# Optimization experiments

Hardware: AMD Instinct MI355X
Metric: run time of the kernel (lower is better)

## Reference

```python
import jax, jax.numpy as jnp
import numpy as np
from jax import lax

K = 7          # kernel size
G = 12         # groups
EPS = 1e-5


def bn(x, gamma, beta, axes):
    # training-mode batch norm (torch default train() mode uses batch stats)
    mean = jnp.mean(x, axis=axes, keepdims=True)
    var = jnp.var(x, axis=axes, keepdims=True)
    shape = [1] * x.ndim
    shape[1 if x.ndim == 4 else -1] = -1
    g = gamma.reshape(shape)
    b = beta.reshape(shape)
    return g * (x - mean) * lax.rsqrt(var + EPS) + b


def setup_inputs() -> dict:
    key = jax.random.key(0)
    ks = jax.random.split(key, 12)
    B, C, H, Wd = 16, 192, 32, 32
    Cr = C // 4                      # reduce_mapping out channels = out_channels // reduce_ratio = 48
    flat = C * H * Wd                # 196608
    inp = {
        "x": jax.random.normal(ks[0], (B, C, H, Wd), jnp.float32),
        "Wr": jax.random.normal(ks[1], (Cr, C), jnp.float32) * 0.05,          # reduce_mapping 1x1 conv
        "gamma_s": jnp.ones((Cr,), jnp.float32),
        "beta_s": jnp.zeros((Cr,), jnp.float32),
        "Ws": jax.random.normal(ks[2], (K * K * G, Cr), jnp.float32) * 0.05,  # span_mapping 1x1 conv
        "W1": jax.random.normal(ks[3], (512, flat), jnp.float32) * 0.002,
        "b1": jnp.zeros((512,), jnp.float32),
        "g1": jnp.ones((512,), jnp.float32),
        "beta1": jnp.zeros((512,), jnp.float32),
        "W2": jax.random.normal(ks[4], (128, 512), jnp.float32) * 0.04,
        "b2": jnp.zeros((128,), jnp.float32),
        "g2": jnp.ones((128,), jnp.float32),
        "beta2": jnp.zeros((128,), jnp.float32),
        "W3": jax.random.normal(ks[5], (17, 128), jnp.float32) * 0.09,
        "b3": jnp.zeros((17,), jnp.float32),
    }
    return inp


def reference(x, Wr, gamma_s, beta_s, Ws, W1, b1, g1, beta1, W2, b2, g2, beta2, W3, b3):
    B, C, H, Wd = x.shape
    Cg = C // G
    # unfold (im2col) with kernel 7, pad 3, stride 1, dil 1 -> [B, C*K*K, H, W]
    # channel ordering (c, kh, kw) matches torch.nn.Unfold
    patches = lax.conv_general_dilated_patches(x, (K, K), (1, 1), [(K // 2, K // 2)] * 2)
    unf = patches.reshape(B, G, Cg, K * K, H, Wd)
    # kernel generation path: 1x1 reduce conv -> BN+ReLU -> 1x1 span conv
    red = jnp.einsum('bchw,oc->bohw', x, Wr)
    red = jax.nn.relu(bn(red, gamma_s, beta_s, (0, 2, 3)))
    ker = jnp.einsum('bchw,oc->bohw', red, Ws).reshape(B, G, K * K, H, Wd)
    # involution: per-pixel kernel multiply + sum over K*K
    out = jnp.einsum('bgkhw,bgckhw->bgchw', ker, unf).reshape(B, C, H, Wd)
    # classifier head
    flat = out.reshape(B, -1)
    h = jax.nn.relu(bn(flat @ W1.T + b1, g1, beta1, (0,)))
    h = jax.nn.relu(bn(h @ W2.T + b2, g2, beta2, (0,)))
    return h @ W3.T + b3
```

## Files before the change

kernel.cpp:

```cpp
#include <hip/hip_runtime.h>

#define EPS 1e-5f

typedef float v4f __attribute__((ext_vector_type(4)));

__global__ __launch_bounds__(256) void k_reduce_conv(
    const float* __restrict__ x, const float* __restrict__ Wr,
    float* __restrict__ red, float* __restrict__ spart)
{
  int ob = blockIdx.x >> 6;
  int pb = blockIdx.x & 63;
  int o0 = ob * 6;
  int pix = (pb << 8) + threadIdx.x;
  int b = pix >> 10;
  int hw = pix & 1023;
  const float* xp = x + ((size_t)b * 192) * 1024 + hw;
  float acc[6] = {0.f, 0.f, 0.f, 0.f, 0.f, 0.f};
  for (int c = 0; c < 192; ++c) {
    float xv = xp[(size_t)c * 1024];
#pragma unroll
    for (int j = 0; j < 6; ++j)
      acc[j] = fmaf(xv, Wr[(o0 + j) * 192 + c], acc[j]);
  }
#pragma unroll
  for (int j = 0; j < 6; ++j)
    red[(size_t)(o0 + j) * 16384 + pix] = acc[j];

  int t = threadIdx.x, lane = t & 63, wid = t >> 6;
  float sv[6], qv[6];
#pragma unroll
  for (int j = 0; j < 6; ++j) { sv[j] = acc[j]; qv[j] = acc[j] * acc[j]; }
#pragma unroll
  for (int off = 32; off > 0; off >>= 1)
#pragma unroll
    for (int j = 0; j < 6; ++j) {
      sv[j] += __shfl_down(sv[j], off);
      qv[j] += __shfl_down(qv[j], off);
    }
  __shared__ float ps[4][12];
  if (lane == 0)
#pragma unroll
    for (int j = 0; j < 6; ++j) { ps[wid][j] = sv[j]; ps[wid][6 + j] = qv[j]; }
  __syncthreads();
  if (t < 12) {
    float v = ps[0][t] + ps[1][t] + ps[2][t] + ps[3][t];
    int j = t % 6, s = t / 6;
    spart[(size_t)(s * 48 + o0 + j) * 64 + pb] = v;
  }
}

__global__ __launch_bounds__(128) void k_stats2(
    const float* __restrict__ spart, float* __restrict__ stats)
{
  int t = threadIdx.x;
  if (t < 96) {
    const v4f* p = (const v4f*)(spart + (size_t)t * 64);
    v4f s = p[0];
#pragma unroll
    for (int i = 1; i < 16; ++i) s += p[i];
    stats[t] = s.x + s.y + s.z + s.w;
  }
}

__global__ __launch_bounds__(256) void k_invol(
    const float* __restrict__ x, const float* __restrict__ red,
    const float* __restrict__ stats, const float* __restrict__ gamma_s,
    const float* __restrict__ beta_s, const float* __restrict__ Ws,
    float* __restrict__ flat)
{
  __shared__ __align__(16) float xt[196 * 20];
  __shared__ __align__(16) float redn[64 * 52];
  __shared__ __align__(16) float kt[49 * 64];

  int bx = blockIdx.x;
  int tile = bx & 15;
  int g = (bx >> 4) % 12;
  int b = bx / 192;
  int th = (tile >> 2) * 8, tw = (tile & 3) * 8;
  int t = threadIdx.x;

  for (int idx = t; idx < 16 * 196; idx += 256) {
    int c = idx / 196, s = idx - c * 196;
    int r = s / 14, q = s - r * 14;
    int sh = th + r - 3, sw = tw + q - 3;
    float v = 0.f;
    if (sh >= 0 && sh < 32 && sw >= 0 && sw < 32)
      v = x[(((size_t)b * 192 + g * 16 + c) << 10) + (sh << 5) + sw];
    xt[s * 20 + c] = v;
  }
  for (int idx = t; idx < 64 * 48; idx += 256) {
    int p = idx & 63, o = idx >> 6;
    int py = p >> 3, px = p & 7;
    float mean = stats[o] * (1.f / 16384.f);
    float var = fmaf(-mean, mean, stats[48 + o] * (1.f / 16384.f));
    float sc = gamma_s[o] * rsqrtf(var + EPS);
    float sh_ = fmaf(-mean, sc, beta_s[o]);
    float v = red[(size_t)o * 16384 + (b << 10) + ((th + py) << 5) + (tw + px)];
    redn[p * 52 + o] = fmaxf(fmaf(v, sc, sh_), 0.f);
  }
  __syncthreads();

  {
    int p = t & 63;
    int kg = __builtin_amdgcn_readfirstlane(t >> 6);
    int k0 = kg * 13;
    float acc[13];
#pragma unroll
    for (int j = 0; j < 13; ++j) acc[j] = 0.f;
    const float* wsp = Ws + (size_t)(g * 49 + k0) * 48;
    for (int o4 = 0; o4 < 48; o4 += 4) {
      v4f rv = *(const v4f*)&redn[p * 52 + o4];
#pragma unroll
      for (int j = 0; j < 13; ++j)
        if (k0 + j < 49) {
          acc[j] = fmaf(rv.x, wsp[j * 48 + o4 + 0], acc[j]);
          acc[j] = fmaf(rv.y, wsp[j * 48 + o4 + 1], acc[j]);
          acc[j] = fmaf(rv.z, wsp[j * 48 + o4 + 2], acc[j]);
          acc[j] = fmaf(rv.w, wsp[j * 48 + o4 + 3], acc[j]);
        }
    }
#pragma unroll
    for (int j = 0; j < 13; ++j)
      if (k0 + j < 49) kt[(k0 + j) * 64 + p] = acc[j];
  }
  __syncthreads();

  {
    int p = t & 63, cq = t >> 6;
    int c0 = cq * 4;
    int py = p >> 3, px = p & 7;
    float a0 = 0.f, a1 = 0.f, a2 = 0.f, a3 = 0.f;
#pragma unroll
    for (int k = 0; k < 49; ++k) {
      int dh = k / 7, dw = k - dh * 7;
      float kv = kt[k * 64 + p];
      const v4f xv = *(const v4f*)&xt[((py + dh) * 14 + px + dw) * 20 + c0];
      a0 = fmaf(kv, xv.x, a0);
      a1 = fmaf(kv, xv.y, a1);
      a2 = fmaf(kv, xv.z, a2);
      a3 = fmaf(kv, xv.w, a3);
    }
    size_t base = (((size_t)b * 192 + g * 16 + c0) << 10) + ((th + py) << 5) + (tw + px);
    flat[base] = a0;
    flat[base + 1024] = a1;
    flat[base + 2048] = a2;
    flat[base + 3072] = a3;
  }
}

__global__ __launch_bounds__(256) void k_gemm1(
    const float* __restrict__ flat, const float* __restrict__ W1,
    float* __restrict__ h1part)
{
  int kc = blockIdx.x;
  int n0 = blockIdx.y * 8;
  int t = threadIdx.x;

  const v4f* W1v = (const v4f*)W1;
  const v4f* flatv = (const v4f*)flat;

  float acc[8][16];
#pragma unroll
  for (int n = 0; n < 8; ++n)
#pragma unroll
    for (int b = 0; b < 16; ++b) acc[n][b] = 0.f;

  int kv = kc * 6144 + t;
  v4f wv[8], wvn[8];
#pragma unroll
  for (int n = 0; n < 8; ++n)
    wv[n] = __builtin_nontemporal_load(&W1v[(size_t)(n0 + n) * 49152 + kv]);

  for (int it = 0; it < 24; ++it) {
    if (it < 23) {
#pragma unroll
      for (int n = 0; n < 8; ++n)
        wvn[n] = __builtin_nontemporal_load(&W1v[(size_t)(n0 + n) * 49152 + kv + 256]);
    }
    v4f fv = flatv[kv];
#pragma unroll
    for (int b = 0; b < 16; ++b) {
      v4f fn;
      if (b < 15) fn = flatv[(size_t)(b + 1) * 49152 + kv];
#pragma unroll
      for (int n = 0; n < 8; ++n) {
        acc[n][b] = fmaf(wv[n].x, fv.x, acc[n][b]);
        acc[n][b] = fmaf(wv[n].y, fv.y, acc[n][b]);
        acc[n][b] = fmaf(wv[n].z, fv.z, acc[n][b]);
        acc[n][b] = fmaf(wv[n].w, fv.w, acc[n][b]);
      }
      fv = fn;
    }
    if (it < 23) {
#pragma unroll
      for (int n = 0; n < 8; ++n) wv[n] = wvn[n];
    }
    kv += 256;
  }

  __shared__ float rbuf[256 * 33];
#pragma unroll
  for (int pass = 0; pass < 4; ++pass) {
    __syncthreads();
#pragma unroll
    for (int nn = 0; nn < 2; ++nn)
#pragma unroll
      for (int b = 0; b < 16; ++b)
        rbuf[t * 33 + nn * 16 + b] = acc[pass * 2 + nn][b];
    __syncthreads();
    int v = t >> 3, i = t & 7;
    float s = 0.f;
#pragma unroll
    for (int j = 0; j < 32; ++j)
      s += rbuf[(i + (j << 3)) * 33 + v];
    s += __shfl_down(s, 4, 8);
    s += __shfl_down(s, 2, 8);
    s += __shfl_down(s, 1, 8);
    if (i == 0) {
      int nn = v >> 4, b = v & 15;
      h1part[(size_t)kc * 8192 + b * 512 + n0 + pass * 2 + nn] = s;
    }
  }
}

__global__ __launch_bounds__(256) void k_bn1(
    const float* __restrict__ h1part, const float* __restrict__ g1,
    const float* __restrict__ beta1, float* __restrict__ h1)
{
  int n = blockIdx.x * 256 + threadIdx.x;
  float v[16];
#pragma unroll
  for (int b = 0; b < 16; ++b) v[b] = 0.f;
#pragma unroll
  for (int y = 0; y < 8; ++y)
#pragma unroll
    for (int b = 0; b < 16; ++b)
      v[b] += h1part[(size_t)y * 8192 + b * 512 + n];
  float s = 0.f;
#pragma unroll
  for (int b = 0; b < 16; ++b) s += v[b];
  float mean = s * (1.f / 16.f);
  float q = 0.f;
#pragma unroll
  for (int b = 0; b < 16; ++b) { float d = v[b] - mean; q = fmaf(d, d, q); }
  float inv = rsqrtf(q * (1.f / 16.f) + EPS);
  float sc = g1[n] * inv, sh = beta1[n];
#pragma unroll
  for (int b = 0; b < 16; ++b)
    h1[b * 512 + n] = fmaxf(fmaf(v[b] - mean, sc, sh), 0.f);
}

__global__ __launch_bounds__(256) void k_gemm2(
    const float* __restrict__ h1, const float* __restrict__ W2,
    float* __restrict__ h2pre)
{
  int gid = blockIdx.x * 256 + threadIdx.x;
  int b = gid >> 7, m = gid & 127;
  const float* hp = h1 + b * 512;
  const float* wp = W2 + m * 512;
  float s = 0.f;
  for (int n = 0; n < 512; n += 4) {
    v4f hv = *(const v4f*)(hp + n);
    v4f wv = *(const v4f*)(wp + n);
    s = fmaf(hv.x, wv.x, s);
    s = fmaf(hv.y, wv.y, s);
    s = fmaf(hv.z, wv.z, s);
    s = fmaf(hv.w, wv.w, s);
  }
  h2pre[b * 128 + m] = s;
}

__global__ __launch_bounds__(320) void k_tail(
    const float* __restrict__ h2pre, const float* __restrict__ g2,
    const float* __restrict__ beta2, const float* __restrict__ W3,
    const float* __restrict__ b3, float* __restrict__ out)
{
  __shared__ float h2[16 * 128];
  int t = threadIdx.x;
  if (t < 128) {
    float v[16];
    float s = 0.f;
#pragma unroll
    for (int b = 0; b < 16; ++b) { v[b] = h2pre[b * 128 + t]; s += v[b]; }
    float mean = s * (1.f / 16.f);
    float q = 0.f;
#pragma unroll
    for (int b = 0; b < 16; ++b) { float d = v[b] - mean; q = fmaf(d, d, q); }
    float inv = rsqrtf(q * (1.f / 16.f) + EPS);
    float sc = g2[t] * inv, sh = beta2[t];
#pragma unroll
    for (int b = 0; b < 16; ++b)
      h2[b * 128 + t] = fmaxf(fmaf(v[b] - mean, sc, sh), 0.f);
  }
  __syncthreads();
  if (t < 272) {
    int b = t / 17, j = t - b * 17;
    float s = b3[j];
    const float* hp = h2 + b * 128;
    const float* wp = W3 + j * 128;
#pragma unroll 4
    for (int m = 0; m < 128; ++m) s = fmaf(hp[m], wp[m], s);
    out[t] = s;
  }
}

extern "C" void kernel_launch(void* const* d_in, const int* in_sizes, int n_in,
                              void* d_out, int out_size, void* d_ws, size_t ws_size,
                              hipStream_t stream)
{
  const float* x       = (const float*)d_in[0];
  const float* Wr      = (const float*)d_in[1];
  const float* gamma_s = (const float*)d_in[2];
  const float* beta_s  = (const float*)d_in[3];
  const float* Ws      = (const float*)d_in[4];
  const float* W1      = (const float*)d_in[5];
  const float* g1      = (const float*)d_in[7];
  const float* beta1   = (const float*)d_in[8];
  const float* W2      = (const float*)d_in[9];
  const float* g2      = (const float*)d_in[11];
  const float* beta2   = (const float*)d_in[12];
  const float* W3      = (const float*)d_in[13];
  const float* b3      = (const float*)d_in[14];

  float* ws = (float*)d_ws;
  float* red    = ws;
  float* flat   = red + 786432;
  float* stats  = flat + 3145728;
  float* spart  = stats + 96;
  float* h1part = spart + 6144;
  float* h1     = h1part + 65536;
  float* h2pre  = h1 + 8192;

  k_reduce_conv<<<512, 256, 0, stream>>>(x, Wr, red, spart);
  k_stats2<<<1, 128, 0, stream>>>(spart, stats);
  k_invol<<<3072, 256, 0, stream>>>(x, red, stats, gamma_s, beta_s, Ws, flat);
  k_gemm1<<<dim3(8, 64), 256, 0, stream>>>(flat, W1, h1part);
  k_bn1<<<2, 256, 0, stream>>>(h1part, g1, beta1, h1);
  k_gemm2<<<8, 256, 0, stream>>>(h1, W2, h2pre);
  k_tail<<<1, 320, 0, stream>>>(h2pre, g2, beta2, W3, b3, (float*)d_out);
}
```

Baseline: 284.4 us.

## Halve gemm1 output tile per block and double-buffer flat and weight loads

The W1 GEMM kernel now computes 4 output neurons per block instead of 8, doubling the grid to 1024 blocks, and declares launch bounds requesting two blocks per SM. All 16 batch rows of flat plus the weights for the next k-step are prefetched into ping-pong register buffers, replacing the per-row software prefetch. This is meant to raise occupancy and hide memory latency on the bandwidth-bound W1 stream. In exchange, the flat activations are read twice as often across blocks, and the larger register buffers may cause pressure or spills.

```diff
diff --git a/kernel.cpp b/kernel.cpp
--- a/kernel.cpp
+++ b/kernel.cpp
@@ -148,59 +148,63 @@
   }
 }
 
-__global__ __launch_bounds__(256) void k_gemm1(
+__global__ __launch_bounds__(256, 2) void k_gemm1(
     const float* __restrict__ flat, const float* __restrict__ W1,
     float* __restrict__ h1part)
 {
   int kc = blockIdx.x;
-  int n0 = blockIdx.y * 8;
+  int n0 = blockIdx.y * 4;
   int t = threadIdx.x;
 
   const v4f* W1v = (const v4f*)W1;
   const v4f* flatv = (const v4f*)flat;
 
-  float acc[8][16];
-#pragma unroll
-  for (int n = 0; n < 8; ++n)
+  float acc[4][16];
+#pragma unroll
+  for (int n = 0; n < 4; ++n)
 #pragma unroll
     for (int b = 0; b < 16; ++b) acc[n][b] = 0.f;
 
   int kv = kc * 6144 + t;
-  v4f wv[8], wvn[8];
-#pragma unroll
-  for (int n = 0; n < 8; ++n)
-    wv[n] = __builtin_nontemporal_load(&W1v[(size_t)(n0 + n) * 49152 + kv]);
-
-  for (int it = 0; it < 24; ++it) {
-    if (it < 23) {
-#pragma unroll
-      for (int n = 0; n < 8; ++n)
-        wvn[n] = __builtin_nontemporal_load(&W1v[(size_t)(n0 + n) * 49152 + kv + 256]);
-    }
-    v4f fv = flatv[kv];
-#pragma unroll
-    for (int b = 0; b < 16; ++b) {
-      v4f fn;
-      if (b < 15) fn = flatv[(size_t)(b + 1) * 49152 + kv];
-#pragma unroll
-      for (int n = 0; n < 8; ++n) {
-        acc[n][b] = fmaf(wv[n].x, fv.x, acc[n][b]);
-        acc[n][b] = fmaf(wv[n].y, fv.y, acc[n][b]);
-        acc[n][b] = fmaf(wv[n].z, fv.z, acc[n][b]);
-        acc[n][b] = fmaf(wv[n].w, fv.w, acc[n][b]);
+
+  v4f fA[16], fB[16], wA[4], wB[4];
+#pragma unroll
+  for (int b = 0; b < 16; ++b) fA[b] = flatv[(size_t)b * 49152 + kv];
+#pragma unroll
+  for (int n = 0; n < 4; ++n)
+    wA[n] = __builtin_nontemporal_load(&W1v[(size_t)(n0 + n) * 49152 + kv]);
+
+  auto phase = [&](v4f (&fC)[16], v4f (&wC)[4], v4f (&fN)[16], v4f (&wN)[4],
+                   bool pre) {
+    if (pre) {
+#pragma unroll
+      for (int b = 0; b < 16; ++b)
+        fN[b] = flatv[(size_t)b * 49152 + kv + 256];
+#pragma unroll
+      for (int n = 0; n < 4; ++n)
+        wN[n] = __builtin_nontemporal_load(
+            &W1v[(size_t)(n0 + n) * 49152 + kv + 256]);
+    }
+#pragma unroll
+    for (int b = 0; b < 16; ++b)
+#pragma unroll
+      for (int n = 0; n < 4; ++n) {
+        acc[n][b] = fmaf(wC[n].x, fC[b].x, acc[n][b]);
+        acc[n][b] = fmaf(wC[n].y, fC[b].y, acc[n][b]);
+        acc[n][b] = fmaf(wC[n].z, fC[b].z, acc[n][b]);
+        acc[n][b] = fmaf(wC[n].w, fC[b].w, acc[n][b]);
       }
-      fv = fn;
-    }
-    if (it < 23) {
-#pragma unroll
-      for (int n = 0; n < 8; ++n) wv[n] = wvn[n];
-    }
     kv += 256;
+  };
+
+  for (int it2 = 0; it2 < 12; ++it2) {
+    phase(fA, wA, fB, wB, true);
+    phase(fB, wB, fA, wA, it2 < 11);
   }
 
   __shared__ float rbuf[256 * 33];
 #pragma unroll
-  for (int pass = 0; pass < 4; ++pass) {
+  for (int pass = 0; pass < 2; ++pass) {
     __syncthreads();
 #pragma unroll
     for (int nn = 0; nn < 2; ++nn)
@@ -334,7 +338,7 @@
   k_reduce_conv<<<512, 256, 0, stream>>>(x, Wr, red, spart);
   k_stats2<<<1, 128, 0, stream>>>(spart, stats);
   k_invol<<<3072, 256, 0, stream>>>(x, red, stats, gamma_s, beta_s, Ws, flat);
-  k_gemm1<<<dim3(8, 64), 256, 0, stream>>>(flat, W1, h1part);
+  k_gemm1<<<dim3(8, 128), 256, 0, stream>>>(flat, W1, h1part);
   k_bn1<<<2, 256, 0, stream>>>(h1part, g1, beta1, h1);
   k_gemm2<<<8, 256, 0, stream>>>(h1, W2, h2pre);
   k_tail<<<1, 320, 0, stream>>>(h2pre, g2, beta2, W3, b3, (float*)d_out);
```

Result: slower. 564.6 us (+98.5%).
